# Kernel optimization log

Measured on AMD Instinct MI355X. Metric: run time of the kernel, lower is better.

Reference implementation:

```python
import jax, jax.numpy as jnp
import numpy as np

C = 1024
CI = 256  # in_channels // inter_ratio
BN_EPS = 1e-5


def setup_inputs() -> dict:
    key = jax.random.key(0)
    ks = jax.random.split(key, 12)
    B, H, W = 16, 64, 32
    xavier = lambda k, o, i: jax.random.uniform(k, (o, i), jnp.float32,
                                                -np.sqrt(6.0 / (o + i)), np.sqrt(6.0 / (o + i)))
    return {
        "x": jax.random.normal(ks[0], (B, C, H, W), jnp.float32),
        "theta_w": xavier(ks[1], CI, C), "theta_b": jnp.zeros((CI,), jnp.float32),
        "phi_w": xavier(ks[2], CI, C), "phi_b": jnp.zeros((CI,), jnp.float32),
        "g_w": xavier(ks[3], CI, C), "g_b": jnp.zeros((CI,), jnp.float32),
        "w_w": xavier(ks[4], C, CI), "w_b": jnp.zeros((C,), jnp.float32),
        # BatchNorm (inference-mode) params; random (not zero-init) so the block is non-trivial
        "bn_gamma": jax.random.normal(ks[5], (C,), jnp.float32) * 0.1 + 1.0,
        "bn_beta": jax.random.normal(ks[6], (C,), jnp.float32) * 0.1,
        "bn_mean": jax.random.normal(ks[7], (C,), jnp.float32) * 0.1,
        "bn_var": jax.random.uniform(ks[8], (C,), jnp.float32, 0.5, 1.5),
    }


def reference(x, theta_w, theta_b, phi_w, phi_b, g_w, g_b, w_w, w_b,
              bn_gamma, bn_beta, bn_mean, bn_var):
    B, Cc, H, W = x.shape
    N = H * W
    xf = x.reshape(B, Cc, N)  # [B, C, N]
    # 1x1 convs == channel GEMMs
    theta = jnp.einsum('oc,bcn->bno', theta_w, xf) + theta_b  # [B, N, Ci]
    phi = jnp.einsum('oc,bcn->bon', phi_w, xf) + phi_b[:, None]  # [B, Ci, N]
    g = jnp.einsum('oc,bcn->bno', g_w, xf) + g_b  # [B, N, Ci]
    attn = jax.nn.softmax(jnp.einsum('bno,bom->bnm', theta, phi), axis=-1)  # [B, N, N]
    y = jnp.einsum('bnm,bmo->bno', attn, g)  # [B, N, Ci]
    z = jnp.einsum('co,bno->bcn', w_w, y) + w_b[None, :, None]  # [B, C, N]
    inv = bn_gamma / jnp.sqrt(bn_var + BN_EPS)
    z = (z - bn_mean[None, :, None]) * inv[None, :, None] + bn_beta[None, :, None]
    return z.reshape(B, Cc, H, W) + x
```

## Files before the change

kernel.cpp:

```cpp
#include <hip/hip_runtime.h>
#include <cstdint>

#define BATCH 16
#define CH 1024
#define CIN 256
#define NSP 2048
#define BN_EPS 1e-5f

typedef _Float16 f16;
typedef f16   f16x8 __attribute__((ext_vector_type(8)));
typedef float f32x4 __attribute__((ext_vector_type(4)));

typedef __attribute__((address_space(3))) void lds_t;
typedef __attribute__((address_space(1))) const void gbl_t;

__device__ __forceinline__ void gld16(void* l, const void* g) {
    __builtin_amdgcn_global_load_lds((gbl_t*)g, (lds_t*)l, 16, 0, 0);
}

__global__ __launch_bounds__(256) void k_prep(
    const float* __restrict__ tw, const float* __restrict__ pw,
    const float* __restrict__ gw, const float* __restrict__ ww,
    const float* __restrict__ wb, const float* __restrict__ gamma,
    const float* __restrict__ beta, const float* __restrict__ mean,
    const float* __restrict__ var,
    f16* __restrict__ w_all, float* __restrict__ inv_out, float* __restrict__ off_out)
{
    int id = blockIdx.x * 256 + threadIdx.x;
    if (id < 4 * 262144) {
        int sel = id >> 18, off = id & 262143;
        const float* src = sel == 0 ? tw : sel == 1 ? pw : sel == 2 ? gw : ww;
        w_all[id] = (f16)src[off];
    } else {
        int c = id - 4 * 262144;
        if (c < CH) {
            float iv = gamma[c] * rsqrtf(var[c] + BN_EPS);
            inv_out[c] = iv;
            off_out[c] = (wb[c] - mean[c]) * iv + beta[c];
        }
    }
}

__global__ __launch_bounds__(256) void k_transpose_x(
    const float* __restrict__ x, f16* __restrict__ xT)
{
    __shared__ float tile[64 * 65];
    int t = threadIdx.x;
    int n0 = blockIdx.x * 64, c0 = blockIdx.y * 64, b = blockIdx.z;
    const float* xb = x + (size_t)b * CH * NSP;
    for (int k = 0; k < 4; ++k) {
        int id = t + 256 * k;
        int row = id >> 4, cc = id & 15;
        float4 v = *(const float4*)(xb + (size_t)(c0 + row) * NSP + n0 + cc * 4);
        tile[row * 65 + cc * 4 + 0] = v.x;
        tile[row * 65 + cc * 4 + 1] = v.y;
        tile[row * 65 + cc * 4 + 2] = v.z;
        tile[row * 65 + cc * 4 + 3] = v.w;
    }
    __syncthreads();
    f16* xTb = xT + (size_t)b * NSP * CH;
    for (int k = 0; k < 2; ++k) {
        int id = t + 256 * k;
        int n = id >> 3, c8 = id & 7;
        f16x8 o;
        #pragma unroll
        for (int j = 0; j < 8; ++j) o[j] = (f16)tile[(c8 * 8 + j) * 65 + n];
        *(f16x8*)(xTb + (size_t)(n0 + n) * CH + c0 + c8 * 8) = o;
    }
}

__global__ __launch_bounds__(256, 3) void k_qkv(
    const f16* __restrict__ xT, const f16* __restrict__ w_all,
    const float* __restrict__ tb, const float* __restrict__ pb,
    const float* __restrict__ gb,
    f16* __restrict__ theta, f16* __restrict__ phiT, f16* __restrict__ gT)
{
    __shared__ char smem[40960];
    f16* a_lds = (f16*)smem;
    f16* b_lds = (f16*)(smem + 8192);
    int t = threadIdx.x;
    int w = t >> 6, lane = t & 63, l15 = lane & 15, q = lane >> 4;
    int sw = l15 & 7;
    int n0 = blockIdx.x * 64, b = blockIdx.y, set = blockIdx.z;
    const f16* W  = w_all + (size_t)set * (CIN * CH);
    const f16* xA = xT + ((size_t)b * NSP + n0) * CH;

    int rA  = lane >> 3;
    int ccs = (lane & 7) ^ rA;

    f32x4 acc[4][4];
    #pragma unroll
    for (int i = 0; i < 4; ++i)
        #pragma unroll
        for (int j = 0; j < 4; ++j) acc[i][j] = (f32x4){0.f, 0.f, 0.f, 0.f};

    for (int it = 0; it < 16; ++it) {
        #pragma unroll
        for (int i = 0; i < 2; ++i) {
            int win = w * 2 + i;
            int n = win * 8 + rA;
            gld16((char*)a_lds + win * 1024,
                  xA + (size_t)n * CH + it * 64 + ccs * 8);
        }
        #pragma unroll
        for (int i = 0; i < 8; ++i) {
            int win = w * 8 + i;
            int o = win * 8 + rA;
            gld16((char*)b_lds + win * 1024,
                  W + (size_t)o * CH + it * 64 + ccs * 8);
        }
        __syncthreads();

        #pragma unroll
        for (int kl = 0; kl < 2; ++kl) {
            int c16 = kl * 4 + q;
            int pos = (c16 ^ sw) & 7;
            f16x8 af[4], bfr[4];
            #pragma unroll
            for (int tn = 0; tn < 4; ++tn)
                af[tn] = *(const f16x8*)(a_lds + (16 * tn + l15) * 64 + pos * 8);
            #pragma unroll
            for (int to = 0; to < 4; ++to)
                bfr[to] = *(const f16x8*)(b_lds + (64 * w + 16 * to + l15) * 64 + pos * 8);
            #pragma unroll
            for (int tn = 0; tn < 4; ++tn)
                #pragma unroll
                for (int to = 0; to < 4; ++to)
                    acc[tn][to] = __builtin_amdgcn_mfma_f32_16x16x32_f16(
                        af[tn], bfr[to], acc[tn][to], 0, 0, 0);
        }
        __syncthreads();
    }

    const float* bias = set == 0 ? tb : set == 1 ? pb : gb;
    float bv[4];
    #pragma unroll
    for (int to = 0; to < 4; ++to) bv[to] = bias[64 * w + 16 * to + l15];

    if (set < 2) {
        f16* e_lds = (f16*)smem;
        #pragma unroll
        for (int tn = 0; tn < 4; ++tn)
            #pragma unroll
            for (int to = 0; to < 4; ++to)
                #pragma unroll
                for (int r = 0; r < 4; ++r)
                    e_lds[(16 * tn + 4 * q + r) * 256 + 64 * w + 16 * to + l15] =
                        (f16)(acc[tn][to][r] + bv[to]);
        __syncthreads();
        f16* dst = (set == 0 ? theta : phiT) + ((size_t)b * NSP + n0) * CIN;
        for (int k2 = 0; k2 < 8; ++k2) {
            int id = t + 256 * k2;
            *(f16x8*)(dst + id * 8) = *(const f16x8*)(e_lds + id * 8);
        }
    } else {
        f16* e_lds = (f16*)smem;
        #pragma unroll
        for (int tn = 0; tn < 4; ++tn)
            #pragma unroll
            for (int to = 0; to < 4; ++to)
                #pragma unroll
                for (int r = 0; r < 4; ++r)
                    e_lds[(64 * w + 16 * to + l15) * 72 + 16 * tn + 4 * q + r] =
                        (f16)(acc[tn][to][r] + bv[to]);
        __syncthreads();
        f16* dst = gT + (size_t)b * CIN * NSP + n0;
        for (int k2 = 0; k2 < 8; ++k2) {
            int id = t + 256 * k2;
            int o = id >> 3, cc = id & 7;
            *(f16x8*)(dst + (size_t)o * NSP + cc * 8) = *(const f16x8*)(e_lds + o * 72 + cc * 8);
        }
    }
}

__global__ __launch_bounds__(256, 2) void k_attn(
    const f16* __restrict__ theta, const f16* __restrict__ phiT,
    const f16* __restrict__ gT, f16* __restrict__ y)
{
    __shared__ char smem[70656];
    f16* p_lds = (f16*)(smem + 65536);
    int t = threadIdx.x;
    int w = t >> 6, lane = t & 63, l15 = lane & 15, q = lane >> 4;
    int n0 = blockIdx.x * 64, b = blockIdx.y;

    f16x8 th[8];
    const f16* thp = theta + ((size_t)b * NSP + n0 + 16 * w + l15) * CIN + q * 8;
    #pragma unroll
    for (int kk = 0; kk < 8; ++kk) th[kk] = *(const f16x8*)(thp + kk * 32);

    f32x4 yacc[16];
    #pragma unroll
    for (int i = 0; i < 16; ++i) yacc[i] = (f32x4){0.f, 0.f, 0.f, 0.f};
    float m_run = -INFINITY, l_run = 0.f;

    const f16* phib = phiT + (size_t)b * NSP * CIN;
    const f16* gTb  = gT + (size_t)b * CIN * NSP;

    int prow_in = lane >> 5;
    int pchunk  = lane & 31;
    int grow_in = lane >> 2;
    int gslot   = lane & 3;

    auto stage = [&](int it, int bufsel) {
        char* pbuf = smem + bufsel * 16384;
        char* gbuf = smem + 32768 + bufsel * 16384;
        const f16* psrc = phib + (size_t)(it * 32) * CIN;
        #pragma unroll
        for (int i = 0; i < 4; ++i) {
            int win = w * 4 + i;
            int row = win * 2 + prow_in;
            int c = (pchunk & 24) | ((pchunk ^ row) & 7);
            gld16(pbuf + win * 1024, psrc + (size_t)row * CIN + c * 8);
        }
        #pragma unroll
        for (int i = 0; i < 4; ++i) {
            int win = w * 4 + i;
            int o = win * 16 + grow_in;
            int c = (gslot ^ o) & 3;
            gld16(gbuf + win * 1024, gTb + (size_t)o * NSP + it * 32 + c * 8);
        }
    };

    stage(0, 0);
    __syncthreads();

    for (int it = 0; it < 64; ++it) {
        int cur = it & 1;
        if (it < 63) stage(it + 1, cur ^ 1);
        const f16* phi_l = (const f16*)(smem + cur * 16384);
        const f16* g_l   = (const f16*)(smem + 32768 + cur * 16384);

        f32x4 sT[2];
        sT[0] = (f32x4){0.f, 0.f, 0.f, 0.f};
        sT[1] = (f32x4){0.f, 0.f, 0.f, 0.f};
        #pragma unroll
        for (int kk = 0; kk < 8; ++kk) {
            int c = kk * 4 + q;
            int pos = (c & 24) | ((c ^ (l15 & 7)) & 7);
            #pragma unroll
            for (int to = 0; to < 2; ++to) {
                f16x8 af = *(const f16x8*)(phi_l + (16 * to + l15) * 256 + pos * 8);
                sT[to] = __builtin_amdgcn_mfma_f32_16x16x32_f16(af, th[kk], sT[to], 0, 0, 0);
            }
        }

        float tm = fmaxf(
            fmaxf(fmaxf(sT[0][0], sT[0][1]), fmaxf(sT[0][2], sT[0][3])),
            fmaxf(fmaxf(sT[1][0], sT[1][1]), fmaxf(sT[1][2], sT[1][3])));
        tm = fmaxf(tm, __shfl_xor(tm, 16));
        tm = fmaxf(tm, __shfl_xor(tm, 32));
        float mnew  = fmaxf(m_run, tm);
        float alpha = __expf(m_run - mnew);
        float rs = 0.f;
        #pragma unroll
        for (int to = 0; to < 2; ++to)
            #pragma unroll
            for (int r = 0; r < 4; ++r) {
                float p = __expf(sT[to][r] - mnew);
                sT[to][r] = p;
                rs += p;
            }
        rs += __shfl_xor(rs, 16);
        rs += __shfl_xor(rs, 32);
        l_run = l_run * alpha + rs;
        m_run = mnew;

        #pragma unroll
        for (int to = 0; to < 2; ++to)
            #pragma unroll
            for (int r = 0; r < 4; ++r)
                p_lds[(16 * w + l15) * 40 + 16 * to + 4 * q + r] = (f16)sT[to][r];

        #pragma unroll
        for (int r = 0; r < 4; ++r) {
            float ar = __shfl(alpha, (lane & 48) | (4 * q + r));
            if (ar != 1.0f) {
                #pragma unroll
                for (int tco = 0; tco < 16; ++tco) yacc[tco][r] *= ar;
            }
        }

        f16x8 pa = *(const f16x8*)(p_lds + (16 * w + l15) * 40 + q * 8);
        int gpos = (q ^ (l15 & 3)) & 3;
        #pragma unroll
        for (int tco = 0; tco < 16; ++tco) {
            f16x8 gfr = *(const f16x8*)(g_l + (16 * tco + l15) * 32 + gpos * 8);
            yacc[tco] = __builtin_amdgcn_mfma_f32_16x16x32_f16(pa, gfr, yacc[tco], 0, 0, 0);
        }

        __syncthreads();
    }

    float linv = 1.0f / l_run;
    f16* e_lds = (f16*)smem;
    #pragma unroll
    for (int r = 0; r < 4; ++r) {
        float iv = __shfl(linv, (lane & 48) | (4 * q + r));
        #pragma unroll
        for (int tco = 0; tco < 16; ++tco)
            e_lds[(16 * w + 4 * q + r) * 256 + 16 * tco + l15] =
                (f16)(yacc[tco][r] * iv);
    }
    __syncthreads();
    f16* dst = y + ((size_t)b * NSP + n0) * CIN;
    for (int k2 = 0; k2 < 8; ++k2) {
        int id = t + 256 * k2;
        *(f16x8*)(dst + id * 8) = *(const f16x8*)(e_lds + id * 8);
    }
}

__global__ __launch_bounds__(256, 3) void k_out(
    const f16* __restrict__ yv, const f16* __restrict__ ww,
    const float* __restrict__ inv, const float* __restrict__ off,
    const float* __restrict__ x, float* __restrict__ out)
{
    __shared__ char smem[40960];
    f16*   a_lds = (f16*)smem;
    f16*   b_lds = (f16*)(smem + 8192);
    float* z_lds = (float*)smem;
    int t = threadIdx.x;
    int w = t >> 6, lane = t & 63, l15 = lane & 15, q = lane >> 4;
    int sw = l15 & 7;
    int n0 = blockIdx.x * 64, cb = blockIdx.y * 256, b = blockIdx.z;

    const f16* yA = yv + ((size_t)b * NSP + n0) * CIN;
    const f16* W  = ww + (size_t)cb * CIN;

    int rA  = lane >> 3;
    int ccs = (lane & 7) ^ rA;

    f32x4 acc[4][4];
    #pragma unroll
    for (int i = 0; i < 4; ++i)
        #pragma unroll
        for (int j = 0; j < 4; ++j) acc[i][j] = (f32x4){0.f, 0.f, 0.f, 0.f};

    for (int it = 0; it < 4; ++it) {
        #pragma unroll
        for (int i = 0; i < 2; ++i) {
            int win = w * 2 + i;
            int n = win * 8 + rA;
            gld16((char*)a_lds + win * 1024,
                  yA + (size_t)n * CIN + it * 64 + ccs * 8);
        }
        #pragma unroll
        for (int i = 0; i < 8; ++i) {
            int win = w * 8 + i;
            int o = win * 8 + rA;
            gld16((char*)b_lds + win * 1024,
                  W + (size_t)o * CIN + it * 64 + ccs * 8);
        }
        __syncthreads();

        #pragma unroll
        for (int kl = 0; kl < 2; ++kl) {
            int c16 = kl * 4 + q;
            int pos = (c16 ^ sw) & 7;
            f16x8 af[4], bfr[4];
            #pragma unroll
            for (int tn = 0; tn < 4; ++tn)
                af[tn] = *(const f16x8*)(a_lds + (16 * tn + l15) * 64 + pos * 8);
            #pragma unroll
            for (int to = 0; to < 4; ++to)
                bfr[to] = *(const f16x8*)(b_lds + (64 * w + 16 * to + l15) * 64 + pos * 8);
            #pragma unroll
            for (int tn = 0; tn < 4; ++tn)
                #pragma unroll
                for (int to = 0; to < 4; ++to)
                    acc[tn][to] = __builtin_amdgcn_mfma_f32_16x16x32_f16(
                        af[tn], bfr[to], acc[tn][to], 0, 0, 0);
        }
        __syncthreads();
    }

    float4 xv[4];
    #pragma unroll
    for (int k2 = 0; k2 < 4; ++k2) {
        int f = t + 256 * k2;
        int zrr = f >> 4, nn4 = f & 15;
        int c = cb + 64 * (zrr >> 4) + (zrr & 15);
        xv[k2] = *(const float4*)(x + ((size_t)b * CH + c) * NSP + n0 + nn4 * 4);
    }

    #pragma unroll
    for (int to = 0; to < 4; ++to) {
        #pragma unroll
        for (int tn = 0; tn < 4; ++tn)
            #pragma unroll
            for (int r = 0; r < 4; ++r)
                z_lds[(16 * w + l15) * 68 + 16 * tn + 4 * q + r] = acc[tn][to][r];
        __syncthreads();

        float4 nxt[4];
        if (to < 3) {
            #pragma unroll
            for (int k2 = 0; k2 < 4; ++k2) {
                int f = t + 256 * k2;
                int zrr = f >> 4, nn4 = f & 15;
                int c = cb + 64 * (zrr >> 4) + 16 * (to + 1) + (zrr & 15);
                nxt[k2] = *(const float4*)(x + ((size_t)b * CH + c) * NSP + n0 + nn4 * 4);
            }
        }

        #pragma unroll
        for (int k2 = 0; k2 < 4; ++k2) {
            int f = t + 256 * k2;
            int zrr = f >> 4, nn4 = f & 15;
            int c = cb + 64 * (zrr >> 4) + 16 * to + (zrr & 15);
            float4 z = *(const float4*)(z_lds + zrr * 68 + nn4 * 4);
            float iv = inv[c], ov = off[c];
            size_t idx = ((size_t)b * CH + c) * NSP + n0 + nn4 * 4;
            float4 o;
            o.x = z.x * iv + ov + xv[k2].x;
            o.y = z.y * iv + ov + xv[k2].y;
            o.z = z.z * iv + ov + xv[k2].z;
            o.w = z.w * iv + ov + xv[k2].w;
            *(float4*)(out + idx) = o;
        }

        if (to < 3) {
            #pragma unroll
            for (int k2 = 0; k2 < 4; ++k2) xv[k2] = nxt[k2];
            __syncthreads();
        }
    }
}

extern "C" void kernel_launch(void* const* d_in, const int* in_sizes, int n_in,
                              void* d_out, int out_size, void* d_ws, size_t ws_size,
                              hipStream_t stream)
{
    const float* x     = (const float*)d_in[0];
    const float* tw    = (const float*)d_in[1];
    const float* tb    = (const float*)d_in[2];
    const float* pw    = (const float*)d_in[3];
    const float* pb    = (const float*)d_in[4];
    const float* gw    = (const float*)d_in[5];
    const float* gb_   = (const float*)d_in[6];
    const float* ww    = (const float*)d_in[7];
    const float* wb    = (const float*)d_in[8];
    const float* gamma = (const float*)d_in[9];
    const float* beta  = (const float*)d_in[10];
    const float* mean  = (const float*)d_in[11];
    const float* var   = (const float*)d_in[12];
    float* out = (float*)d_out;

    char* ws = (char*)d_ws;
    f16* xT    = (f16*)ws;
    f16* theta = (f16*)(ws + 67108864);
    f16* phiT  = (f16*)(ws + 83886080);
    f16* gT    = (f16*)(ws + 100663296);
    f16* yv    = (f16*)(ws + 117440512);
    f16* w_all = (f16*)(ws + 134217728);
    float* inv  = (float*)(ws + 136314880);
    float* offv = (float*)(ws + 136318976);

    k_prep<<<4100, 256, 0, stream>>>(tw, pw, gw, ww, wb, gamma, beta, mean, var,
                                     w_all, inv, offv);
    k_transpose_x<<<dim3(32, 16, 16), 256, 0, stream>>>(x, xT);
    k_qkv<<<dim3(32, 16, 3), 256, 0, stream>>>(xT, w_all, tb, pb, gb_, theta, phiT, gT);
    k_attn<<<dim3(32, 16), 256, 0, stream>>>(theta, phiT, gT, yv);
    k_out<<<dim3(32, 4, 16), 256, 0, stream>>>(yv, w_all + 3 * 262144, inv, offv, x, out);
}
```

Before: 483.8 us.

## Stage g tiles through registers into padded LDS and reorder attention grid

The g (value) tile is no longer copied straight into LDS with global_load_lds and an XOR swizzle. It is now loaded into registers one iteration ahead and written into a padded (stride 40) LDS buffer after the softmax, so the MFMA reads avoid swizzle arithmetic and bank conflicts. The grid is transposed so consecutive blocks share a batch index across different query tiles, which may improve L2 reuse of phi and g. P stores are packed into 4-wide f16 writes. LDS use grows and register pressure rises from the extra g staging registers, which could hurt occupancy at 2 blocks per CU.

```diff
diff --git a/kernel.cpp b/kernel.cpp
--- a/kernel.cpp
+++ b/kernel.cpp
@@ -8,6 +8,7 @@
 #define BN_EPS 1e-5f
 
 typedef _Float16 f16;
+typedef f16   f16x4 __attribute__((ext_vector_type(4)));
 typedef f16   f16x8 __attribute__((ext_vector_type(8)));
 typedef float f32x4 __attribute__((ext_vector_type(4)));
 
@@ -177,11 +178,11 @@
     const f16* __restrict__ theta, const f16* __restrict__ phiT,
     const f16* __restrict__ gT, f16* __restrict__ y)
 {
-    __shared__ char smem[70656];
-    f16* p_lds = (f16*)(smem + 65536);
+    __shared__ char smem[78848];
+    f16* p_lds = (f16*)(smem + 73728);
     int t = threadIdx.x;
     int w = t >> 6, lane = t & 63, l15 = lane & 15, q = lane >> 4;
-    int n0 = blockIdx.x * 64, b = blockIdx.y;
+    int b = blockIdx.x, n0 = blockIdx.y * 64;
 
     f16x8 th[8];
     const f16* thp = theta + ((size_t)b * NSP + n0 + 16 * w + l15) * CIN + q * 8;
@@ -198,12 +199,8 @@
 
     int prow_in = lane >> 5;
     int pchunk  = lane & 31;
-    int grow_in = lane >> 2;
-    int gslot   = lane & 3;
-
-    auto stage = [&](int it, int bufsel) {
-        char* pbuf = smem + bufsel * 16384;
-        char* gbuf = smem + 32768 + bufsel * 16384;
+    auto stage_phi = [&](int it, int sel) {
+        char* pbuf = smem + sel * 16384;
         const f16* psrc = phib + (size_t)(it * 32) * CIN;
         #pragma unroll
         for (int i = 0; i < 4; ++i) {
@@ -212,23 +209,36 @@
             int c = (pchunk & 24) | ((pchunk ^ row) & 7);
             gld16(pbuf + win * 1024, psrc + (size_t)row * CIN + c * 8);
         }
-        #pragma unroll
-        for (int i = 0; i < 4; ++i) {
-            int win = w * 4 + i;
-            int o = win * 16 + grow_in;
-            int c = (gslot ^ o) & 3;
-            gld16(gbuf + win * 1024, gTb + (size_t)o * NSP + it * 32 + c * 8);
-        }
     };
 
-    stage(0, 0);
+    int go = t >> 2;
+    int gc = t & 3;
+    f16x8 gr[4];
+    auto load_g = [&](int it) {
+        #pragma unroll
+        for (int i = 0; i < 4; ++i)
+            gr[i] = *(const f16x8*)(gTb + (size_t)(i * 64 + go) * NSP + it * 32 + gc * 8);
+    };
+    auto write_g = [&](int sel) {
+        f16* gb = (f16*)(smem + 32768 + sel * 20480);
+        #pragma unroll
+        for (int i = 0; i < 4; ++i)
+            *(f16x8*)(gb + (i * 64 + go) * 40 + gc * 8) = gr[i];
+    };
+
+    load_g(0);
+    stage_phi(0, 0);
+    write_g(0);
     __syncthreads();
 
     for (int it = 0; it < 64; ++it) {
         int cur = it & 1;
-        if (it < 63) stage(it + 1, cur ^ 1);
+        if (it < 63) {
+            load_g(it + 1);
+            stage_phi(it + 1, cur ^ 1);
+        }
         const f16* phi_l = (const f16*)(smem + cur * 16384);
-        const f16* g_l   = (const f16*)(smem + 32768 + cur * 16384);
+        const f16* g_l   = (const f16*)(smem + 32768 + cur * 20480);
 
         f32x4 sT[2];
         sT[0] = (f32x4){0.f, 0.f, 0.f, 0.f};
@@ -266,10 +276,10 @@
         m_run = mnew;
 
         #pragma unroll
-        for (int to = 0; to < 2; ++to)
-            #pragma unroll
-            for (int r = 0; r < 4; ++r)
-                p_lds[(16 * w + l15) * 40 + 16 * to + 4 * q + r] = (f16)sT[to][r];
+        for (int to = 0; to < 2; ++to) {
+            f16x4 pk = { (f16)sT[to][0], (f16)sT[to][1], (f16)sT[to][2], (f16)sT[to][3] };
+            *(f16x4*)(p_lds + (16 * w + l15) * 40 + 16 * to + 4 * q) = pk;
+        }
 
         #pragma unroll
         for (int r = 0; r < 4; ++r) {
@@ -280,11 +290,12 @@
             }
         }
 
+        if (it < 63) write_g(cur ^ 1);
+
         f16x8 pa = *(const f16x8*)(p_lds + (16 * w + l15) * 40 + q * 8);
-        int gpos = (q ^ (l15 & 3)) & 3;
         #pragma unroll
         for (int tco = 0; tco < 16; ++tco) {
-            f16x8 gfr = *(const f16x8*)(g_l + (16 * tco + l15) * 32 + gpos * 8);
+            f16x8 gfr = *(const f16x8*)(g_l + (16 * tco + l15) * 40 + q * 8);
             yacc[tco] = __builtin_amdgcn_mfma_f32_16x16x32_f16(pa, gfr, yacc[tco], 0, 0, 0);
         }
 
@@ -459,6 +470,6 @@
                                      w_all, inv, offv);
     k_transpose_x<<<dim3(32, 16, 16), 256, 0, stream>>>(x, xT);
     k_qkv<<<dim3(32, 16, 3), 256, 0, stream>>>(xT, w_all, tb, pb, gb_, theta, phiT, gT);
-    k_attn<<<dim3(32, 16), 256, 0, stream>>>(theta, phiT, gT, yv);
+    k_attn<<<dim3(16, 32), 256, 0, stream>>>(theta, phiT, gT, yv);
     k_out<<<dim3(32, 4, 16), 256, 0, stream>>>(yv, w_all + 3 * 262144, inv, offv, x, out);
 }
```

Result: no change. 479.7 us (-0.8%).

## Restructure attention kernel around 32x32 MFMA tiles with split-key warps

Applied to the files above, without the earlier changes.

Rewrites the flash-attention kernel to use 32x32x16 MFMA instructions. Each warp handles a 32-query by 32-key score tile, with two warps splitting the 64-key block, and tiles grow to 64 keys per iteration so there are half as many loop steps. Row max and sum are combined across warps through LDS, and the output accumulation splits the CIN dimension across warps. The double-buffered prefetch is replaced by single buffers refilled between barriers, and the grid is reordered so batch is the fast index. This adds extra barriers per iteration and loses the overlap between loading and compute.

```diff
diff --git a/kernel.cpp b/kernel.cpp
--- a/kernel.cpp
+++ b/kernel.cpp
@@ -8,8 +8,10 @@
 #define BN_EPS 1e-5f
 
 typedef _Float16 f16;
+typedef f16   f16x4 __attribute__((ext_vector_type(4)));
 typedef f16   f16x8 __attribute__((ext_vector_type(8)));
 typedef float f32x4 __attribute__((ext_vector_type(4)));
+typedef float f32x16 __attribute__((ext_vector_type(16)));
 
 typedef __attribute__((address_space(3))) void lds_t;
 typedef __attribute__((address_space(1))) const void gbl_t;
@@ -177,136 +179,182 @@
     const f16* __restrict__ theta, const f16* __restrict__ phiT,
     const f16* __restrict__ gT, f16* __restrict__ y)
 {
-    __shared__ char smem[70656];
-    f16* p_lds = (f16*)(smem + 65536);
+    __shared__ char smem[76544];
+    f16* phi_lds = (f16*)smem;
+    f16* g_lds   = (f16*)(smem + 32768);
+    f16* p_lds   = (f16*)(smem + 65536);
+    float* pmax_lds  = (float*)(smem + 75264);
+    float* psum_lds  = (float*)(smem + 75776);
+    float* alpha_lds = (float*)(smem + 76288);
+
     int t = threadIdx.x;
-    int w = t >> 6, lane = t & 63, l15 = lane & 15, q = lane >> 4;
-    int n0 = blockIdx.x * 64, b = blockIdx.y;
-
-    f16x8 th[8];
-    const f16* thp = theta + ((size_t)b * NSP + n0 + 16 * w + l15) * CIN + q * 8;
-    #pragma unroll
-    for (int kk = 0; kk < 8; ++kk) th[kk] = *(const f16x8*)(thp + kk * 32);
-
-    f32x4 yacc[16];
-    #pragma unroll
-    for (int i = 0; i < 16; ++i) yacc[i] = (f32x4){0.f, 0.f, 0.f, 0.f};
-    float m_run = -INFINITY, l_run = 0.f;
-
+    int w = t >> 6, lane = t & 63;
+    int l31 = lane & 31, hi = lane >> 5;
+    int qh = w & 1, kh = w >> 1;
+    int b = blockIdx.x, n0 = blockIdx.y * 64;
+
+    const f16* thb  = theta + (size_t)b * NSP * CIN;
     const f16* phib = phiT + (size_t)b * NSP * CIN;
     const f16* gTb  = gT + (size_t)b * CIN * NSP;
 
-    int prow_in = lane >> 5;
-    int pchunk  = lane & 31;
-    int grow_in = lane >> 2;
-    int gslot   = lane & 3;
-
-    auto stage = [&](int it, int bufsel) {
-        char* pbuf = smem + bufsel * 16384;
-        char* gbuf = smem + 32768 + bufsel * 16384;
-        const f16* psrc = phib + (size_t)(it * 32) * CIN;
-        #pragma unroll
-        for (int i = 0; i < 4; ++i) {
-            int win = w * 4 + i;
-            int row = win * 2 + prow_in;
-            int c = (pchunk & 24) | ((pchunk ^ row) & 7);
-            gld16(pbuf + win * 1024, psrc + (size_t)row * CIN + c * 8);
-        }
-        #pragma unroll
-        for (int i = 0; i < 4; ++i) {
-            int win = w * 4 + i;
-            int o = win * 16 + grow_in;
-            int c = (gslot ^ o) & 3;
-            gld16(gbuf + win * 1024, gTb + (size_t)o * NSP + it * 32 + c * 8);
-        }
-    };
-
-    stage(0, 0);
+    f16x8 th[16];
+    {
+        const f16* tp = thb + (size_t)(n0 + qh * 32 + l31) * CIN + 8 * hi;
+        #pragma unroll
+        for (int s = 0; s < 16; ++s) th[s] = *(const f16x8*)(tp + s * 16);
+    }
+
+    f32x16 acc[2][2];
+    #pragma unroll
+    for (int i = 0; i < 2; ++i)
+        #pragma unroll
+        for (int j = 0; j < 2; ++j)
+            #pragma unroll
+            for (int r = 0; r < 16; ++r) acc[i][j][r] = 0.f;
+    float m_run = -INFINITY, l_run = 0.f;
+
+    int p_cdst = lane & 31;
+    int g_rin = lane >> 3, g_cdst = lane & 7;
+
+    #define DMA_PHI(IT)                                                         \
+        _Pragma("unroll")                                                       \
+        for (int i_ = 0; i_ < 8; ++i_) {                                        \
+            int win_ = w * 8 + i_;                                              \
+            int row_ = win_ * 2 + hi;                                           \
+            int cs_ = (p_cdst & 24) | ((p_cdst ^ row_) & 7);                    \
+            gld16((char*)phi_lds + win_ * 1024,                                 \
+                  phib + (size_t)((IT) * 64 + row_) * CIN + cs_ * 8);           \
+        }
+    #define DMA_G(IT)                                                           \
+        _Pragma("unroll")                                                       \
+        for (int i_ = 0; i_ < 8; ++i_) {                                        \
+            int win_ = w * 8 + i_;                                              \
+            int row_ = win_ * 8 + g_rin;                                        \
+            int cs_ = g_cdst ^ (row_ & 7);                                      \
+            gld16((char*)g_lds + win_ * 1024,                                   \
+                  gTb + (size_t)row_ * NSP + (IT) * 64 + cs_ * 8);              \
+        }
+
+    DMA_PHI(0)
+    DMA_G(0)
     __syncthreads();
 
-    for (int it = 0; it < 64; ++it) {
-        int cur = it & 1;
-        if (it < 63) stage(it + 1, cur ^ 1);
-        const f16* phi_l = (const f16*)(smem + cur * 16384);
-        const f16* g_l   = (const f16*)(smem + 32768 + cur * 16384);
-
-        f32x4 sT[2];
-        sT[0] = (f32x4){0.f, 0.f, 0.f, 0.f};
-        sT[1] = (f32x4){0.f, 0.f, 0.f, 0.f};
-        #pragma unroll
-        for (int kk = 0; kk < 8; ++kk) {
-            int c = kk * 4 + q;
-            int pos = (c & 24) | ((c ^ (l15 & 7)) & 7);
-            #pragma unroll
-            for (int to = 0; to < 2; ++to) {
-                f16x8 af = *(const f16x8*)(phi_l + (16 * to + l15) * 256 + pos * 8);
-                sT[to] = __builtin_amdgcn_mfma_f32_16x16x32_f16(af, th[kk], sT[to], 0, 0, 0);
+    int srow = kh * 32 + l31;
+    int qrow = qh * 32 + l31;
+    int mli  = kh * 64 + qrow;
+
+    for (int it = 0; it < 32; ++it) {
+        f32x16 sacc;
+        #pragma unroll
+        for (int r = 0; r < 16; ++r) sacc[r] = 0.f;
+        #pragma unroll
+        for (int s = 0; s < 16; ++s) {
+            int ch = 2 * s + hi;
+            int slot = (ch & 24) | ((ch ^ srow) & 7);
+            f16x8 af = *(const f16x8*)(phi_lds + srow * 256 + slot * 8);
+            sacc = __builtin_amdgcn_mfma_f32_32x32x16_f16(af, th[s], sacc, 0, 0, 0);
+        }
+
+        float tmax = sacc[0];
+        #pragma unroll
+        for (int r = 1; r < 16; ++r) tmax = fmaxf(tmax, sacc[r]);
+        tmax = fmaxf(tmax, __shfl_xor(tmax, 32));
+        if (lane < 32) pmax_lds[mli] = tmax;
+        __syncthreads();
+
+        float tile_max = fmaxf(tmax, pmax_lds[mli ^ 64]);
+        float mnew  = fmaxf(m_run, tile_max);
+        float alpha = __expf(m_run - mnew);
+        m_run = mnew;
+        float rs = 0.f;
+        float pv[16];
+        #pragma unroll
+        for (int r = 0; r < 16; ++r) {
+            pv[r] = __expf(sacc[r] - mnew);
+            rs += pv[r];
+        }
+        rs += __shfl_xor(rs, 32);
+        if (lane < 32) {
+            psum_lds[mli] = rs;
+            if (kh == 0) alpha_lds[qrow] = alpha;
+        }
+        #pragma unroll
+        for (int g4 = 0; g4 < 4; ++g4) {
+            f16x4 pk = { (f16)pv[4*g4+0], (f16)pv[4*g4+1], (f16)pv[4*g4+2], (f16)pv[4*g4+3] };
+            *(f16x4*)(p_lds + qrow * 76 + kh * 32 + 8 * g4 + 4 * hi) = pk;
+        }
+        __syncthreads();
+
+        if (it < 31) DMA_PHI(it + 1)
+
+        l_run = l_run * alpha + rs + psum_lds[mli ^ 64];
+
+        f32x4 av[2][4];
+        float mn = 1.0f;
+        #pragma unroll
+        for (int Mt = 0; Mt < 2; ++Mt)
+            #pragma unroll
+            for (int g4 = 0; g4 < 4; ++g4) {
+                av[Mt][g4] = *(const f32x4*)(alpha_lds + Mt * 32 + 8 * g4 + 4 * hi);
+                mn = fminf(mn, fminf(fminf(av[Mt][g4][0], av[Mt][g4][1]),
+                                     fminf(av[Mt][g4][2], av[Mt][g4][3])));
             }
-        }
-
-        float tm = fmaxf(
-            fmaxf(fmaxf(sT[0][0], sT[0][1]), fmaxf(sT[0][2], sT[0][3])),
-            fmaxf(fmaxf(sT[1][0], sT[1][1]), fmaxf(sT[1][2], sT[1][3])));
-        tm = fmaxf(tm, __shfl_xor(tm, 16));
-        tm = fmaxf(tm, __shfl_xor(tm, 32));
-        float mnew  = fmaxf(m_run, tm);
-        float alpha = __expf(m_run - mnew);
-        float rs = 0.f;
-        #pragma unroll
-        for (int to = 0; to < 2; ++to)
-            #pragma unroll
-            for (int r = 0; r < 4; ++r) {
-                float p = __expf(sT[to][r] - mnew);
-                sT[to][r] = p;
-                rs += p;
+        if (__any(mn < 1.0f)) {
+            #pragma unroll
+            for (int Mt = 0; Mt < 2; ++Mt)
+                #pragma unroll
+                for (int g4 = 0; g4 < 4; ++g4)
+                    #pragma unroll
+                    for (int rr = 0; rr < 4; ++rr) {
+                        acc[Mt][0][4*g4+rr] *= av[Mt][g4][rr];
+                        acc[Mt][1][4*g4+rr] *= av[Mt][g4][rr];
+                    }
+        }
+
+        #pragma unroll
+        for (int ks = 0; ks < 4; ++ks) {
+            f16x8 pa0 = *(const f16x8*)(p_lds + l31 * 76 + ks * 16 + 8 * hi);
+            f16x8 pa1 = *(const f16x8*)(p_lds + (32 + l31) * 76 + ks * 16 + 8 * hi);
+            int slot = (2 * ks + hi) ^ (l31 & 7);
+            f16x8 gb0 = *(const f16x8*)(g_lds + (64 * w + l31) * 64 + slot * 8);
+            f16x8 gb1 = *(const f16x8*)(g_lds + (64 * w + 32 + l31) * 64 + slot * 8);
+            acc[0][0] = __builtin_amdgcn_mfma_f32_32x32x16_f16(pa0, gb0, acc[0][0], 0, 0, 0);
+            acc[0][1] = __builtin_amdgcn_mfma_f32_32x32x16_f16(pa0, gb1, acc[0][1], 0, 0, 0);
+            acc[1][0] = __builtin_amdgcn_mfma_f32_32x32x16_f16(pa1, gb0, acc[1][0], 0, 0, 0);
+            acc[1][1] = __builtin_amdgcn_mfma_f32_32x32x16_f16(pa1, gb1, acc[1][1], 0, 0, 0);
+        }
+        __syncthreads();
+
+        if (it < 31) DMA_G(it + 1)
+    }
+
+    if (lane < 32 && kh == 0) alpha_lds[qrow] = 1.0f / l_run;
+    __syncthreads();
+    f16* e_lds = (f16*)smem;
+    #pragma unroll
+    for (int Mt = 0; Mt < 2; ++Mt)
+        #pragma unroll
+        for (int g4 = 0; g4 < 4; ++g4) {
+            f32x4 lv = *(const f32x4*)(alpha_lds + Mt * 32 + 8 * g4 + 4 * hi);
+            #pragma unroll
+            for (int rr = 0; rr < 4; ++rr) {
+                int q = Mt * 32 + 8 * g4 + 4 * hi + rr;
+                #pragma unroll
+                for (int Nt = 0; Nt < 2; ++Nt) {
+                    int cin = 64 * w + Nt * 32 + l31;
+                    e_lds[q * 264 + cin] = (f16)(acc[Mt][Nt][4*g4+rr] * lv[rr]);
+                }
             }
-        rs += __shfl_xor(rs, 16);
-        rs += __shfl_xor(rs, 32);
-        l_run = l_run * alpha + rs;
-        m_run = mnew;
-
-        #pragma unroll
-        for (int to = 0; to < 2; ++to)
-            #pragma unroll
-            for (int r = 0; r < 4; ++r)
-                p_lds[(16 * w + l15) * 40 + 16 * to + 4 * q + r] = (f16)sT[to][r];
-
-        #pragma unroll
-        for (int r = 0; r < 4; ++r) {
-            float ar = __shfl(alpha, (lane & 48) | (4 * q + r));
-            if (ar != 1.0f) {
-                #pragma unroll
-                for (int tco = 0; tco < 16; ++tco) yacc[tco][r] *= ar;
-            }
-        }
-
-        f16x8 pa = *(const f16x8*)(p_lds + (16 * w + l15) * 40 + q * 8);
-        int gpos = (q ^ (l15 & 3)) & 3;
-        #pragma unroll
-        for (int tco = 0; tco < 16; ++tco) {
-            f16x8 gfr = *(const f16x8*)(g_l + (16 * tco + l15) * 32 + gpos * 8);
-            yacc[tco] = __builtin_amdgcn_mfma_f32_16x16x32_f16(pa, gfr, yacc[tco], 0, 0, 0);
-        }
-
-        __syncthreads();
-    }
-
-    float linv = 1.0f / l_run;
-    f16* e_lds = (f16*)smem;
-    #pragma unroll
-    for (int r = 0; r < 4; ++r) {
-        float iv = __shfl(linv, (lane & 48) | (4 * q + r));
-        #pragma unroll
-        for (int tco = 0; tco < 16; ++tco)
-            e_lds[(16 * w + 4 * q + r) * 256 + 16 * tco + l15] =
-                (f16)(yacc[tco][r] * iv);
-    }
+        }
     __syncthreads();
     f16* dst = y + ((size_t)b * NSP + n0) * CIN;
     for (int k2 = 0; k2 < 8; ++k2) {
         int id = t + 256 * k2;
-        *(f16x8*)(dst + id * 8) = *(const f16x8*)(e_lds + id * 8);
-    }
+        int row = id >> 5, cc = id & 31;
+        *(f16x8*)(dst + (size_t)row * CIN + cc * 8) = *(const f16x8*)(e_lds + row * 264 + cc * 8);
+    }
+    #undef DMA_PHI
+    #undef DMA_G
 }
 
 __global__ __launch_bounds__(256, 3) void k_out(
@@ -459,6 +507,6 @@
                                      w_all, inv, offv);
     k_transpose_x<<<dim3(32, 16, 16), 256, 0, stream>>>(x, xT);
     k_qkv<<<dim3(32, 16, 3), 256, 0, stream>>>(xT, w_all, tb, pb, gb_, theta, phiT, gT);
-    k_attn<<<dim3(32, 16), 256, 0, stream>>>(theta, phiT, gT, yv);
+    k_attn<<<dim3(16, 32), 256, 0, stream>>>(theta, phiT, gT, yv);
     k_out<<<dim3(32, 4, 16), 256, 0, stream>>>(yv, w_all + 3 * 262144, inv, offv, x, out);
 }
```

Result: no change. 480.4 us (-0.7%).
